# Performance work log

Measured on AMD Instinct MI355X. Metric: run time of the kernel, lower is better.

The kernel has to match this reference:

```python
import jax, jax.numpy as jnp
import numpy as np

ALPHA = 0.2  # LeakyReLU negative slope


def setup_inputs() -> dict:
    key = jax.random.key(0)
    k1, k2, k3, k4 = jax.random.split(key, 4)
    B, T, D_in, H, S = 32, 1024, 64, 64, 2
    embedding = jax.random.normal(k1, (B, T, D_in), dtype=jnp.float32)
    x = jax.random.normal(k2, (S * B, T, D_in), dtype=jnp.float32)
    # xavier_uniform-ish scale for params
    W = jax.random.normal(k3, (D_in, H), dtype=jnp.float32) * (1.414 * np.sqrt(2.0 / (D_in + H)))
    a = jax.random.normal(k4, (2 * H, 1), dtype=jnp.float32) * (1.414 * np.sqrt(2.0 / (2 * H + 1)))
    return {"embedding": embedding, "x": x, "W": W, "a": a, "input_size": S}


def reference(embedding, x, W, a, input_size):
    # embedding: [B, T, D_in], W: [D_in, H], a: [2H, 1], x: [S*B, T, D_in]
    H = W.shape[1]
    h = jnp.einsum("btd,dh->bth", embedding, W)          # [B, T, H]
    a1 = a[:H, 0]                                        # attends to h_i (query side)
    a2 = a[H:, 0]                                        # attends to h_j (key side)
    f1 = h @ a1                                          # [B, T]
    f2 = h @ a2                                          # [B, T]
    # e_ij = leakyrelu(a1.h_i + a2.h_j) -- avoids materializing [B,T,T,2H]
    e = jax.nn.leaky_relu(f1[:, :, None] + f2[:, None, :], negative_slope=ALPHA)  # [B, T, T]
    attn = jax.nn.softmax(e, axis=2)                     # [B, T, T]
    attn_tiled = jnp.tile(attn, (input_size, 1, 1))      # [S*B, T, T] (dropout: eval mode, identity)
    out = jnp.einsum("bij,bjd->bid", attn_tiled, x)      # [S*B, T, D_in]
    return out
```

## Files before the change

kernel.cpp:

```cpp
#include <hip/hip_runtime.h>

typedef float  f32x4 __attribute__((ext_vector_type(4)));
typedef _Float16 h16x8 __attribute__((ext_vector_type(8)));
typedef _Float16 h16x2 __attribute__((ext_vector_type(2)));

#define LOG2E 1.4426950408889634f
#define ALPHA 0.2f

__device__ __forceinline__ float fexp2(float v) {
#if __has_builtin(__builtin_amdgcn_exp2f)
  return __builtin_amdgcn_exp2f(v);
#else
  return exp2f(v);
#endif
}

__global__ __launch_bounds__(256) void fkern(
    const float* __restrict__ emb, const float* __restrict__ W,
    const float* __restrict__ a, float* __restrict__ f1, float* __restrict__ f2)
{
  __shared__ float w1s[64], w2s[64];
  const int t = threadIdx.x;
  if (t < 128) {
    const int d = t & 63;
    const float* wrow = W + d * 64;
    const float* av = a + (t >> 6) * 64;
    float s = 0.f;
#pragma unroll
    for (int h = 0; h < 64; ++h) s = fmaf(wrow[h], av[h], s);
    if (t < 64) w1s[d] = s; else w2s[d] = s;
  }
  __syncthreads();
  const int R = blockIdx.x * 64 + (t >> 2);
  const int q = t & 3;
  const f32x4* er = (const f32x4*)(emb + (size_t)R * 64 + q * 16);
  float s1 = 0.f, s2 = 0.f;
#pragma unroll
  for (int r = 0; r < 4; ++r) {
    f32x4 v = er[r];
#pragma unroll
    for (int c = 0; c < 4; ++c) {
      s1 = fmaf(v[c], w1s[q * 16 + r * 4 + c], s1);
      s2 = fmaf(v[c], w2s[q * 16 + r * 4 + c], s2);
    }
  }
  s1 += __shfl_xor(s1, 1); s1 += __shfl_xor(s1, 2);
  s2 += __shfl_xor(s2, 1); s2 += __shfl_xor(s2, 2);
  if (q == 0) { f1[R] = s1 * LOG2E; f2[R] = s2 * LOG2E; }
}

__global__ __launch_bounds__(256, 1) void attn_main(
    const float* __restrict__ x, const float* __restrict__ f1g,
    const float* __restrict__ f2g, float* __restrict__ out)
{
  __shared__ __attribute__((aligned(16))) _Float16 Xt[2][128 * 136];
  __shared__ float f2s[1024];
  __shared__ float Zs[128];
  __shared__ float red[4];

  const int t    = threadIdx.x;
  const int wid  = t >> 6;
  const int lane = t & 63;
  const int l15  = lane & 15;
  const int g    = lane >> 4;
  const int b    = blockIdx.x >> 3;
  const int brow = (blockIdx.x & 7) * 128;

  {
    f32x4 v = *(const f32x4*)(f2g + b * 1024 + t * 4);
    *(f32x4*)(f2s + t * 4) = v;
    float m = fmaxf(fmaxf(v[0], v[1]), fmaxf(v[2], v[3]));
#pragma unroll
    for (int off = 1; off < 64; off <<= 1) m = fmaxf(m, __shfl_xor(m, off));
    if (lane == 0) red[wid] = m;
  }

  const float f1v0 = f1g[b * 1024 + brow + wid * 32 + l15];
  const float f1v1 = f1g[b * 1024 + brow + wid * 32 + 16 + l15];

  float rv[64];

  auto stage_loads = [&](int kc) {
#pragma unroll
    for (int p = 0; p < 8; ++p) {
      const int pp = wid * 8 + p;
      const int h  = pp >> 4;
      const int j0 = (pp & 15) * 8;
      const float* base = x + (size_t)(b + 32 * h) * 65536
                            + (size_t)(kc * 128 + j0 + 2 * g) * 64 + l15;
#pragma unroll
      for (int i = 0; i < 4; ++i) {
        rv[p * 8 + i]     = base[i * 16];
        rv[p * 8 + 4 + i] = base[64 + i * 16];
      }
    }
  };
  auto stage_writes = [&](int buf) {
#pragma unroll
    for (int p = 0; p < 8; ++p) {
      const int pp = wid * 8 + p;
      const int h  = pp >> 4;
      const int k  = (pp & 15) * 8 + 2 * g;
#pragma unroll
      for (int i = 0; i < 4; ++i) {
        const int row = h * 64 + l15 + 16 * i;
        h16x2 hp;
        hp[0] = (_Float16)rv[p * 8 + i];
        hp[1] = (_Float16)rv[p * 8 + 4 + i];
        *(unsigned*)&Xt[buf][row * 136 + k] = __builtin_bit_cast(unsigned, hp);
      }
    }
  };

  stage_loads(0);
  __syncthreads();
  const float mf2 = fmaxf(fmaxf(red[0], red[1]), fmaxf(red[2], red[3]));
  float A0, B0, A1, B1;
  { const float u = f1v0 + mf2; const float mL = fmaxf(u, ALPHA * u);
    A0 = f1v0 - mL; B0 = fmaf(ALPHA, f1v0, -mL); }
  { const float u = f1v1 + mf2; const float mL = fmaxf(u, ALPHA * u);
    A1 = f1v1 - mL; B1 = fmaf(ALPHA, f1v1, -mL); }
  stage_writes(0);
  __syncthreads();

  f32x4 acc[2][8] = {};
  float z0 = 0.f, z1 = 0.f;

  for (int kc = 0; kc < 8; ++kc) {
    const int buf = kc & 1;
    if (kc < 7) stage_loads(kc + 1);
#pragma unroll
    for (int ks = 0; ks < 4; ++ks) {
      const int jb = kc * 128 + ks * 32 + g * 8;
      f32x4 f2a = *(const f32x4*)(f2s + jb);
      f32x4 f2b = *(const f32x4*)(f2s + jb + 4);
      float fv[8];
#pragma unroll
      for (int i = 0; i < 4; ++i) { fv[i] = f2a[i]; fv[4 + i] = f2b[i]; }
      h16x8 a0, a1;
#pragma unroll
      for (int jj = 0; jj < 4; ++jj) {
        const float fA = fv[2 * jj], fB = fv[2 * jj + 1];
        float p00 = fexp2(fmaxf(A0 + fA, fmaf(ALPHA, fA, B0)));
        float p01 = fexp2(fmaxf(A0 + fB, fmaf(ALPHA, fB, B0)));
        h16x2 pk0 = __builtin_bit_cast(h16x2, __builtin_amdgcn_cvt_pkrtz(p00, p01));
        a0[2 * jj] = pk0[0]; a0[2 * jj + 1] = pk0[1];
        z0 += (float)pk0[0] + (float)pk0[1];
        float p10 = fexp2(fmaxf(A1 + fA, fmaf(ALPHA, fA, B1)));
        float p11 = fexp2(fmaxf(A1 + fB, fmaf(ALPHA, fB, B1)));
        h16x2 pk1 = __builtin_bit_cast(h16x2, __builtin_amdgcn_cvt_pkrtz(p10, p11));
        a1[2 * jj] = pk1[0]; a1[2 * jj + 1] = pk1[1];
        z1 += (float)pk1[0] + (float)pk1[1];
      }
#pragma unroll
      for (int nf = 0; nf < 8; ++nf) {
        h16x8 bf = *(const h16x8*)&Xt[buf][(nf * 16 + l15) * 136 + ks * 32 + g * 8];
        acc[0][nf] = __builtin_amdgcn_mfma_f32_16x16x32_f16(a0, bf, acc[0][nf], 0, 0, 0);
        acc[1][nf] = __builtin_amdgcn_mfma_f32_16x16x32_f16(a1, bf, acc[1][nf], 0, 0, 0);
      }
    }
    if (kc < 7) stage_writes(buf ^ 1);
    __syncthreads();
  }

  z0 += __shfl_xor(z0, 16); z0 += __shfl_xor(z0, 32);
  z1 += __shfl_xor(z1, 16); z1 += __shfl_xor(z1, 32);
  if (lane < 16) { Zs[wid * 32 + lane] = z0; Zs[wid * 32 + 16 + lane] = z1; }
  __syncthreads();
  float rz0[4], rz1[4];
#pragma unroll
  for (int r = 0; r < 4; ++r) {
    rz0[r] = 1.0f / Zs[wid * 32 + g * 4 + r];
    rz1[r] = 1.0f / Zs[wid * 32 + 16 + g * 4 + r];
  }
  const int i0 = brow + wid * 32;
#pragma unroll
  for (int nf = 0; nf < 8; ++nf) {
    const int n  = nf * 16 + l15;
    const int bo = b + ((n >= 64) ? 32 : 0);
    float* op = out + (size_t)bo * 65536 + (n & 63);
#pragma unroll
    for (int r = 0; r < 4; ++r) {
      op[(size_t)(i0 + g * 4 + r) * 64]      = acc[0][nf][r] * rz0[r];
      op[(size_t)(i0 + 16 + g * 4 + r) * 64] = acc[1][nf][r] * rz1[r];
    }
  }
}

extern "C" void kernel_launch(void* const* d_in, const int* in_sizes, int n_in,
                              void* d_out, int out_size, void* d_ws, size_t ws_size,
                              hipStream_t stream) {
  const float* emb = (const float*)d_in[0];
  const float* x   = (const float*)d_in[1];
  const float* W   = (const float*)d_in[2];
  const float* a   = (const float*)d_in[3];
  float* f1 = (float*)d_ws;
  float* f2 = f1 + 32 * 1024;
  fkern<<<512, 256, 0, stream>>>(emb, W, a, f1, f2);
  attn_main<<<256, 256, 0, stream>>>(x, f1, f2, (float*)d_out);
}
```

Before: 39.63 us.

## Split attention output columns across 8 waves and compute row sums via MFMA

Doubles the block to 512 threads (8 waves). Each pair of waves shares the same 32 query rows but takes a different 64-column half of the output, so every wave carries half as many accumulators and staging registers. The softmax denominators are now accumulated with an extra MFMA against a vector of ones instead of scalar adds plus shuffles and shared-memory reduction. This aims to hide latency better on each CU with more waves, at the cost of each wave pair recomputing the same exponentials.

```diff
diff --git a/kernel.cpp b/kernel.cpp
--- a/kernel.cpp
+++ b/kernel.cpp
@@ -49,13 +49,12 @@
   if (q == 0) { f1[R] = s1 * LOG2E; f2[R] = s2 * LOG2E; }
 }
 
-__global__ __launch_bounds__(256, 1) void attn_main(
+__global__ __launch_bounds__(512, 1) void attn_main(
     const float* __restrict__ x, const float* __restrict__ f1g,
     const float* __restrict__ f2g, float* __restrict__ out)
 {
   __shared__ __attribute__((aligned(16))) _Float16 Xt[2][128 * 136];
   __shared__ float f2s[1024];
-  __shared__ float Zs[128];
   __shared__ float red[4];
 
   const int t    = threadIdx.x;
@@ -63,10 +62,12 @@
   const int lane = t & 63;
   const int l15  = lane & 15;
   const int g    = lane >> 4;
+  const int wc   = wid & 1;
+  const int wr   = wid >> 1;
   const int b    = blockIdx.x >> 3;
   const int brow = (blockIdx.x & 7) * 128;
 
-  {
+  if (t < 256) {
     f32x4 v = *(const f32x4*)(f2g + b * 1024 + t * 4);
     *(f32x4*)(f2s + t * 4) = v;
     float m = fmaxf(fmaxf(v[0], v[1]), fmaxf(v[2], v[3]));
@@ -75,15 +76,15 @@
     if (lane == 0) red[wid] = m;
   }
 
-  const float f1v0 = f1g[b * 1024 + brow + wid * 32 + l15];
-  const float f1v1 = f1g[b * 1024 + brow + wid * 32 + 16 + l15];
-
-  float rv[64];
+  const float f1v0 = f1g[b * 1024 + brow + wr * 32 + l15];
+  const float f1v1 = f1g[b * 1024 + brow + wr * 32 + 16 + l15];
+
+  float rv[32];
 
   auto stage_loads = [&](int kc) {
 #pragma unroll
-    for (int p = 0; p < 8; ++p) {
-      const int pp = wid * 8 + p;
+    for (int p = 0; p < 4; ++p) {
+      const int pp = wid * 4 + p;
       const int h  = pp >> 4;
       const int j0 = (pp & 15) * 8;
       const float* base = x + (size_t)(b + 32 * h) * 65536
@@ -97,8 +98,8 @@
   };
   auto stage_writes = [&](int buf) {
 #pragma unroll
-    for (int p = 0; p < 8; ++p) {
-      const int pp = wid * 8 + p;
+    for (int p = 0; p < 4; ++p) {
+      const int pp = wid * 4 + p;
       const int h  = pp >> 4;
       const int k  = (pp & 15) * 8 + 2 * g;
 #pragma unroll
@@ -123,8 +124,11 @@
   stage_writes(0);
   __syncthreads();
 
-  f32x4 acc[2][8] = {};
-  float z0 = 0.f, z1 = 0.f;
+  f32x4 acc[2][4] = {};
+  f32x4 accz[2] = {};
+  h16x8 ones;
+#pragma unroll
+  for (int i = 0; i < 8; ++i) ones[i] = (_Float16)1.0f;
 
   for (int kc = 0; kc < 8; ++kc) {
     const int buf = kc & 1;
@@ -145,38 +149,34 @@
         float p01 = fexp2(fmaxf(A0 + fB, fmaf(ALPHA, fB, B0)));
         h16x2 pk0 = __builtin_bit_cast(h16x2, __builtin_amdgcn_cvt_pkrtz(p00, p01));
         a0[2 * jj] = pk0[0]; a0[2 * jj + 1] = pk0[1];
-        z0 += (float)pk0[0] + (float)pk0[1];
         float p10 = fexp2(fmaxf(A1 + fA, fmaf(ALPHA, fA, B1)));
         float p11 = fexp2(fmaxf(A1 + fB, fmaf(ALPHA, fB, B1)));
         h16x2 pk1 = __builtin_bit_cast(h16x2, __builtin_amdgcn_cvt_pkrtz(p10, p11));
         a1[2 * jj] = pk1[0]; a1[2 * jj + 1] = pk1[1];
-        z1 += (float)pk1[0] + (float)pk1[1];
-      }
-#pragma unroll
-      for (int nf = 0; nf < 8; ++nf) {
-        h16x8 bf = *(const h16x8*)&Xt[buf][(nf * 16 + l15) * 136 + ks * 32 + g * 8];
+      }
+#pragma unroll
+      for (int nf = 0; nf < 4; ++nf) {
+        h16x8 bf = *(const h16x8*)&Xt[buf][(wc * 64 + nf * 16 + l15) * 136 + ks * 32 + g * 8];
         acc[0][nf] = __builtin_amdgcn_mfma_f32_16x16x32_f16(a0, bf, acc[0][nf], 0, 0, 0);
         acc[1][nf] = __builtin_amdgcn_mfma_f32_16x16x32_f16(a1, bf, acc[1][nf], 0, 0, 0);
       }
+      accz[0] = __builtin_amdgcn_mfma_f32_16x16x32_f16(a0, ones, accz[0], 0, 0, 0);
+      accz[1] = __builtin_amdgcn_mfma_f32_16x16x32_f16(a1, ones, accz[1], 0, 0, 0);
     }
     if (kc < 7) stage_writes(buf ^ 1);
     __syncthreads();
   }
 
-  z0 += __shfl_xor(z0, 16); z0 += __shfl_xor(z0, 32);
-  z1 += __shfl_xor(z1, 16); z1 += __shfl_xor(z1, 32);
-  if (lane < 16) { Zs[wid * 32 + lane] = z0; Zs[wid * 32 + 16 + lane] = z1; }
-  __syncthreads();
   float rz0[4], rz1[4];
 #pragma unroll
   for (int r = 0; r < 4; ++r) {
-    rz0[r] = 1.0f / Zs[wid * 32 + g * 4 + r];
-    rz1[r] = 1.0f / Zs[wid * 32 + 16 + g * 4 + r];
-  }
-  const int i0 = brow + wid * 32;
-#pragma unroll
-  for (int nf = 0; nf < 8; ++nf) {
-    const int n  = nf * 16 + l15;
+    rz0[r] = 1.0f / accz[0][r];
+    rz1[r] = 1.0f / accz[1][r];
+  }
+  const int i0 = brow + wr * 32;
+#pragma unroll
+  for (int nf = 0; nf < 4; ++nf) {
+    const int n  = wc * 64 + nf * 16 + l15;
     const int bo = b + ((n >= 64) ? 32 : 0);
     float* op = out + (size_t)bo * 65536 + (n & 63);
 #pragma unroll
@@ -197,5 +197,5 @@
   float* f1 = (float*)d_ws;
   float* f2 = f1 + 32 * 1024;
   fkern<<<512, 256, 0, stream>>>(emb, W, a, f1, f2);
-  attn_main<<<256, 256, 0, stream>>>(x, f1, f2, (float*)d_out);
-}
+  attn_main<<<256, 512, 0, stream>>>(x, f1, f2, (float*)d_out);
+}
```

Measured after the change: 37.76 us. -4.7%, faster.
